# Kernel tuning notes

Hardware: AMD Instinct MI355X
Metric: run time of the kernel (lower is better)

Reference implementation:

```python
import jax, jax.numpy as jnp
import numpy as np

PS = 16
E = 512          # embed_dim
H = 8            # num_heads
EPS = 1e-5


def _ln(x, g, b):
    m = jnp.mean(x, axis=-1, keepdims=True)
    v = jnp.mean((x - m) ** 2, axis=-1, keepdims=True)
    return (x - m) * jax.lax.rsqrt(v + EPS) * g + b


def _mha(q_in, kv_in, in_w, in_b, out_w, out_b):
    # torch nn.MultiheadAttention: packed in_proj [3E, E], out_proj [E, E]
    Bq, Lq, _ = q_in.shape
    Lk = kv_in.shape[1]
    d = E // H
    wq, wk, wv = jnp.split(in_w, 3, axis=0)
    bq, bk, bv = jnp.split(in_b, 3, axis=0)
    q = (q_in @ wq.T + bq).reshape(Bq, Lq, H, d)
    k = (kv_in @ wk.T + bk).reshape(Bq, Lk, H, d)
    v = (kv_in @ wv.T + bv).reshape(Bq, Lk, H, d)
    scores = jnp.einsum('bqhd,bkhd->bhqk', q, k) / jnp.sqrt(jnp.float32(d))
    a = jax.nn.softmax(scores, axis=-1)
    o = jnp.einsum('bhqk,bkhd->bqhd', a, v).reshape(Bq, Lq, E)
    return o @ out_w.T + out_b


def setup_inputs() -> dict:
    key = jax.random.key(0)
    ks = jax.random.split(key, 24)
    s = 0.02
    D = 3 * PS * PS
    inp = {
        'neighbor_patches': jax.random.normal(ks[0], (8, 32, 32, 9, 3, PS, PS), jnp.float32),
        'w_pe': jax.random.normal(ks[1], (E, D), jnp.float32) * s,
        'b_pe': jnp.zeros((E,), jnp.float32),
        'pos_embed': jax.random.normal(ks[2], (1, 9, E), jnp.float32),
        'sa_in_w': jax.random.normal(ks[3], (3 * E, E), jnp.float32) * s,
        'sa_in_b': jnp.zeros((3 * E,), jnp.float32),
        'sa_out_w': jax.random.normal(ks[4], (E, E), jnp.float32) * s,
        'sa_out_b': jnp.zeros((E,), jnp.float32),
        'g1': jnp.ones((E,), jnp.float32), 'beta1': jnp.zeros((E,), jnp.float32),
        'ca_in_w': jax.random.normal(ks[5], (3 * E, E), jnp.float32) * s,
        'ca_in_b': jnp.zeros((3 * E,), jnp.float32),
        'ca_out_w': jax.random.normal(ks[6], (E, E), jnp.float32) * s,
        'ca_out_b': jnp.zeros((E,), jnp.float32),
        'g2': jnp.ones((E,), jnp.float32), 'beta2': jnp.zeros((E,), jnp.float32),
        'w1': jax.random.normal(ks[7], (4 * E, E), jnp.float32) * s,
        'b1': jnp.zeros((4 * E,), jnp.float32),
        'w2': jax.random.normal(ks[8], (E, 4 * E), jnp.float32) * s,
        'b2': jnp.zeros((E,), jnp.float32),
        'g3': jnp.ones((E,), jnp.float32), 'beta3': jnp.zeros((E,), jnp.float32),
    }
    return inp


def reference(neighbor_patches, w_pe, b_pe, pos_embed,
              sa_in_w, sa_in_b, sa_out_w, sa_out_b, g1, beta1,
              ca_in_w, ca_in_b, ca_out_w, ca_out_b, g2, beta2,
              w1, b1, w2, b2, g3, beta3):
    B, NH, NW, NN, C, ps, _ = neighbor_patches.shape
    x = neighbor_patches.reshape(B * NH * NW, NN, C * ps * ps)
    x = x @ w_pe.T + b_pe                       # [BN, 9, E]
    x = x + pos_embed
    attn = _mha(x, x, sa_in_w, sa_in_b, sa_out_w, sa_out_b)
    x = _ln(x + attn, g1, beta1)
    cq = x[:, 4:5, :]                            # center query [BN, 1, E]
    attn = _mha(cq, x, ca_in_w, ca_in_b, ca_out_w, ca_out_b)
    c = _ln(cq + attn, g2, beta2)
    ffn = jax.nn.gelu(c @ w1.T + b1, approximate=False) @ w2.T + b2
    out = _ln(c + ffn, g3, beta3)
    return out[:, 0, :].reshape(B, NH * NW, E)
```

## Files before the change

kernel.cpp:

```cpp
#include <hip/hip_runtime.h>


typedef unsigned short u16;
typedef u16   u16x8 __attribute__((ext_vector_type(8)));
typedef u16   u16x4 __attribute__((ext_vector_type(4)));
typedef __bf16 bf16x8 __attribute__((ext_vector_type(8)));
typedef float f32x4 __attribute__((ext_vector_type(4)));

static __device__ __forceinline__ u16 f2bf(float f) {
  union { float f; unsigned u; } v; v.f = f;
  unsigned r = v.u + 0x7FFFu + ((v.u >> 16) & 1u);
  return (u16)(r >> 16);
}
static __device__ __forceinline__ float bf2f(u16 u) {
  union { unsigned u; float f; } v; v.u = ((unsigned)u) << 16;
  return v.f;
}

static __device__ __forceinline__ void gld16(const void* g, void* l) {
  __builtin_amdgcn_global_load_lds(
      (__attribute__((address_space(1))) unsigned int*)(size_t)g,
      (__attribute__((address_space(3))) unsigned int*)(unsigned)(size_t)l,
      16, 0, 0);
}

static __device__ __forceinline__ int xcd_swz(int bid, int nwg) {
  int q = nwg >> 3, r = nwg & 7;
  int xcd = bid & 7, sub = bid >> 3;
  return (xcd < r ? xcd * (q + 1) : r * (q + 1) + (xcd - r) * q) + sub;
}

#define BAR   __builtin_amdgcn_s_barrier()
#define VM0   asm volatile("s_waitcnt vmcnt(0)" ::: "memory")
#define VM4   asm volatile("s_waitcnt vmcnt(4)" ::: "memory")

template<bool HAS_POS, bool HAS_RES, bool HAS_GELU>
__global__ __launch_bounds__(256, 3) void gemm_k2(
    const u16* __restrict__ A, int lda,
    const u16* __restrict__ W,
    const float* __restrict__ bias,
    const float* __restrict__ pos,
    const u16* res, int res_stride,
    u16* out,
    int M, int N, int K, int nbx)
{
  __shared__ u16 As[3][4096];
  __shared__ u16 Bs[3][4096];

  const int t    = threadIdx.x;
  const int lane = t & 63, wv = t >> 6;
  const int swz  = xcd_swz(blockIdx.x, gridDim.x);
  const int bm   = (swz / nbx) * 128, bn = (swz % nbx) * 128;
  const int wr   = wv >> 1, wc = wv & 1;

  const int srow = lane >> 2;
  const int skk  = (((lane & 3) ^ ((lane >> 3) & 3)) << 3);
  const int lr = lane & 15;
  const int rg = (((lane >> 4) ^ ((lr >> 1) & 3)) << 3);

  f32x4 acc[4][4] = {};

  auto stage = [&](int buf, int kt) {
    #pragma unroll
    for (int c = 0; c < 2; ++c) {
      int rr = (wv + 4 * c) * 16 + srow;
      gld16(A + (size_t)(bm + rr) * lda + kt * 32 + skk, &As[buf][(wv + 4 * c) * 512]);
      gld16(W + (size_t)(bn + rr) * K   + kt * 32 + skk, &Bs[buf][(wv + 4 * c) * 512]);
    }
  };

  const int nkt = K >> 5;
  stage(0, 0);
  stage(1, 1);
  VM4; BAR;

  int cur = 0, st = 2;
  for (int kt = 0; kt < nkt; ++kt) {
    if (kt + 2 < nkt) stage(st, kt + 2);

    bf16x8 a[4], b[4];
    #pragma unroll
    for (int m = 0; m < 4; ++m) {
      int row = wr * 64 + m * 16 + lr;
      a[m] = *(const bf16x8*)&As[cur][row * 32 + rg];
    }
    #pragma unroll
    for (int n = 0; n < 4; ++n) {
      int row = wc * 64 + n * 16 + lr;
      b[n] = *(const bf16x8*)&Bs[cur][row * 32 + rg];
    }
    #pragma unroll
    for (int m = 0; m < 4; ++m)
      #pragma unroll
      for (int n = 0; n < 4; ++n)
        acc[m][n] = __builtin_amdgcn_mfma_f32_16x16x32_bf16(a[m], b[n], acc[m][n], 0, 0, 0);

    if (kt + 2 < nkt) { VM4; } else { VM0; }
    BAR;
    cur = (cur == 2) ? 0 : cur + 1;
    st  = (st  == 2) ? 0 : st  + 1;
  }

  const int lq = lane >> 4;
  #pragma unroll
  for (int m = 0; m < 4; ++m) {
    #pragma unroll
    for (int n = 0; n < 4; ++n) {
      int col = bn + wc * 64 + n * 16 + lr;
      float bv = bias[col];
      #pragma unroll
      for (int r = 0; r < 4; ++r) {
        int row = bm + wr * 64 + m * 16 + lq * 4 + r;
        float v = acc[m][n][r] + bv;
        if constexpr (HAS_POS) v += pos[(row % 9) * 512 + col];
        if constexpr (HAS_RES) v += bf2f(res[(size_t)row * res_stride + col]);
        if constexpr (HAS_GELU) v = 0.5f * v * (1.f + erff(v * 0.70710678118f));
        out[(size_t)row * N + col] = f2bf(v);
      }
    }
  }
}

__global__ __launch_bounds__(256) void ln_k(
    const u16* in,
    const float* __restrict__ g, const float* __restrict__ be,
    u16* out_bf, float* out_f32, int rows)
{
  int wv = threadIdx.x >> 6, lane = threadIdx.x & 63;
  int row = blockIdx.x * 4 + wv;
  if (row >= rows) return;
  const u16* p = in + (size_t)row * 512;
  u16x8 v = *(const u16x8*)&p[lane * 8];
  float x[8], s = 0.f, sq = 0.f;
  #pragma unroll
  for (int j = 0; j < 8; ++j) { x[j] = bf2f(v[j]); s += x[j]; sq += x[j] * x[j]; }
  #pragma unroll
  for (int o = 32; o > 0; o >>= 1) { s += __shfl_xor(s, o, 64); sq += __shfl_xor(sq, o, 64); }
  float mean = s * (1.f / 512.f);
  float var  = sq * (1.f / 512.f) - mean * mean;
  float rs   = rsqrtf(var + 1e-5f);
  float y[8];
  #pragma unroll
  for (int j = 0; j < 8; ++j) {
    int c = lane * 8 + j;
    y[j] = (x[j] - mean) * rs * g[c] + be[c];
  }
  if (out_bf) {
    u16x8 o8;
    #pragma unroll
    for (int j = 0; j < 8; ++j) o8[j] = f2bf(y[j]);
    *(u16x8*)&out_bf[(size_t)row * 512 + lane * 8] = o8;
  }
  if (out_f32) {
    #pragma unroll
    for (int j = 0; j < 8; ++j) out_f32[(size_t)row * 512 + lane * 8 + j] = y[j];
  }
}

__global__ __launch_bounds__(256) void sa_attn_k(const u16* __restrict__ qkv,
                                                 u16* __restrict__ out)
{
  __shared__ u16  s_qkv[9 * 1536];
  __shared__ float s_sc[8][81];
  const int s = blockIdx.x, t = threadIdx.x;
  const u16* src = qkv + (size_t)s * 9 * 1536;
  for (int i = t; i < (9 * 1536) / 8; i += 256)
    *(u16x8*)&s_qkv[i * 8] = *(const u16x8*)&src[i * 8];
  __syncthreads();

  const int h = t >> 5, sl = t & 31;
  for (int p = sl; p < 81; p += 32) {
    int qi = p / 9, ki = p % 9;
    const u16* qp = &s_qkv[qi * 1536 + h * 64];
    const u16* kp = &s_qkv[ki * 1536 + 512 + h * 64];
    float d = 0.f;
    #pragma unroll
    for (int e8 = 0; e8 < 8; ++e8) {
      u16x8 qv = *(const u16x8*)&qp[e8 * 8];
      u16x8 kv = *(const u16x8*)&kp[e8 * 8];
      #pragma unroll
      for (int j = 0; j < 8; ++j) d += bf2f(qv[j]) * bf2f(kv[j]);
    }
    s_sc[h][p] = d * 0.125f;
  }
  __syncthreads();

  if (t < 72) {
    int hh = t / 9, qi = t % 9;
    float* sc = &s_sc[hh][qi * 9];
    float mx = sc[0];
    #pragma unroll
    for (int i = 1; i < 9; ++i) mx = fmaxf(mx, sc[i]);
    float e[9], sum = 0.f;
    #pragma unroll
    for (int i = 0; i < 9; ++i) { e[i] = __expf(sc[i] - mx); sum += e[i]; }
    float inv = 1.f / sum;
    #pragma unroll
    for (int i = 0; i < 9; ++i) sc[i] = e[i] * inv;
  }
  __syncthreads();

  for (int gidx = sl; gidx < 72; gidx += 32) {
    int qi = gidx >> 3, dg = gidx & 7;
    float a[8] = {};
    #pragma unroll
    for (int ki = 0; ki < 9; ++ki) {
      float pr = s_sc[h][qi * 9 + ki];
      u16x8 vv = *(const u16x8*)&s_qkv[ki * 1536 + 1024 + h * 64 + dg * 8];
      #pragma unroll
      for (int j = 0; j < 8; ++j) a[j] += pr * bf2f(vv[j]);
    }
    u16x8 o8;
    #pragma unroll
    for (int j = 0; j < 8; ++j) o8[j] = f2bf(a[j]);
    *(u16x8*)&out[((size_t)s * 9 + qi) * 512 + h * 64 + dg * 8] = o8;
  }
}

__global__ __launch_bounds__(256) void ca_attn_k(const u16* __restrict__ q,
                                                 const u16* __restrict__ kv,
                                                 u16* __restrict__ out)
{
  __shared__ u16  s_q[512];
  __shared__ u16  s_kv[9 * 1024];
  __shared__ float s_sc[8][9];
  const int s = blockIdx.x, t = threadIdx.x;
  if (t < 64) *(u16x8*)&s_q[t * 8] = *(const u16x8*)&q[(size_t)s * 512 + t * 8];
  for (int i = t; i < (9 * 1024) / 8; i += 256)
    *(u16x8*)&s_kv[i * 8] = *(const u16x8*)&kv[(size_t)s * 9 * 1024 + i * 8];
  __syncthreads();

  if (t < 72) {
    int h = t / 9, ki = t % 9;
    const u16* qp = &s_q[h * 64];
    const u16* kp = &s_kv[ki * 1024 + h * 64];
    float d = 0.f;
    #pragma unroll
    for (int e8 = 0; e8 < 8; ++e8) {
      u16x8 qv = *(const u16x8*)&qp[e8 * 8];
      u16x8 kvv = *(const u16x8*)&kp[e8 * 8];
      #pragma unroll
      for (int j = 0; j < 8; ++j) d += bf2f(qv[j]) * bf2f(kvv[j]);
    }
    s_sc[h][ki] = d * 0.125f;
  }
  __syncthreads();

  if (t < 8) {
    float* sc = s_sc[t];
    float mx = sc[0];
    #pragma unroll
    for (int i = 1; i < 9; ++i) mx = fmaxf(mx, sc[i]);
    float e[9], sum = 0.f;
    #pragma unroll
    for (int i = 0; i < 9; ++i) { e[i] = __expf(sc[i] - mx); sum += e[i]; }
    float inv = 1.f / sum;
    #pragma unroll
    for (int i = 0; i < 9; ++i) sc[i] = e[i] * inv;
  }
  __syncthreads();

  if (t < 64) {
    int h = t >> 3, dg = t & 7;
    float a[8] = {};
    #pragma unroll
    for (int ki = 0; ki < 9; ++ki) {
      float pr = s_sc[h][ki];
      u16x8 vv = *(const u16x8*)&s_kv[ki * 1024 + 512 + h * 64 + dg * 8];
      #pragma unroll
      for (int j = 0; j < 8; ++j) a[j] += pr * bf2f(vv[j]);
    }
    u16x8 o8;
    #pragma unroll
    for (int j = 0; j < 8; ++j) o8[j] = f2bf(a[j]);
    *(u16x8*)&out[(size_t)s * 512 + h * 64 + dg * 8] = o8;
  }
}

__global__ __launch_bounds__(256) void cvt_k(const float* __restrict__ in,
                                             u16* __restrict__ out, long n)
{
  long i = ((long)blockIdx.x * 256 + threadIdx.x) * 4;
  long stride = (long)gridDim.x * 1024;
  for (; i < n; i += stride) {
    float4 f = *(const float4*)&in[i];
    u16x4 o; o.x = f2bf(f.x); o.y = f2bf(f.y); o.z = f2bf(f.z); o.w = f2bf(f.w);
    *(u16x4*)&out[i] = o;
  }
}

extern "C" void kernel_launch(void* const* d_in, const int* in_sizes, int n_in,
                              void* d_out, int out_size, void* d_ws, size_t ws_size,
                              hipStream_t stream)
{
  const float* patches  = (const float*)d_in[0];
  const float* w_pe     = (const float*)d_in[1];
  const float* b_pe     = (const float*)d_in[2];
  const float* pos      = (const float*)d_in[3];
  const float* sa_in_w  = (const float*)d_in[4];
  const float* sa_in_b  = (const float*)d_in[5];
  const float* sa_out_w = (const float*)d_in[6];
  const float* sa_out_b = (const float*)d_in[7];
  const float* g1       = (const float*)d_in[8];
  const float* beta1    = (const float*)d_in[9];
  const float* ca_in_w  = (const float*)d_in[10];
  const float* ca_in_b  = (const float*)d_in[11];
  const float* ca_out_w = (const float*)d_in[12];
  const float* ca_out_b = (const float*)d_in[13];
  const float* g2       = (const float*)d_in[14];
  const float* beta2    = (const float*)d_in[15];
  const float* w1       = (const float*)d_in[16];
  const float* b1       = (const float*)d_in[17];
  const float* w2       = (const float*)d_in[18];
  const float* b2       = (const float*)d_in[19];
  const float* g3       = (const float*)d_in[20];
  const float* beta3    = (const float*)d_in[21];
  float* out = (float*)d_out;

  char* base = (char*)d_ws;
  u16* wbf        = (u16*)base;
  u16* w_pe_bf    = wbf;
  u16* sa_in_bf   = wbf + 393216;
  u16* sa_out_bf  = wbf + 1179648;
  u16* ca_in_bf   = wbf + 1441792;
  u16* ca_out_bf  = wbf + 2228224;
  u16* w1_bf      = wbf + 2490368;
  u16* w2_bf      = wbf + 3538944;
  u16* x_bf  = (u16*)(base + 9175040ull);
  u16* qkv   = (u16*)(base + 84672512ull);
  u16* pat_bf = qkv;
  u16* sattn = (u16*)(base + 311164928ull);
  u16* q_bf  = (u16*)(base + 386662400ull);
  u16* cattn = (u16*)(base + 395051008ull);
  u16* csum  = (u16*)(base + 403439616ull);
  u16* h_bf  = (u16*)(base + 411828224ull);
  u16* osum  = (u16*)(base + 445382656ull);

  cvt_k<<<2048, 256, 0, stream>>>(patches, pat_bf, 56623104L);
  cvt_k<<<384, 256, 0, stream>>>(w_pe, w_pe_bf, 393216L);
  cvt_k<<<768, 256, 0, stream>>>(sa_in_w, sa_in_bf, 786432L);
  cvt_k<<<256, 256, 0, stream>>>(sa_out_w, sa_out_bf, 262144L);
  cvt_k<<<768, 256, 0, stream>>>(ca_in_w, ca_in_bf, 786432L);
  cvt_k<<<256, 256, 0, stream>>>(ca_out_w, ca_out_bf, 262144L);
  cvt_k<<<1024, 256, 0, stream>>>(w1, w1_bf, 1048576L);
  cvt_k<<<1024, 256, 0, stream>>>(w2, w2_bf, 1048576L);

  gemm_k2<true, false, false><<<2304, 256, 0, stream>>>(
      pat_bf, 768, w_pe_bf, b_pe, pos, nullptr, 0, x_bf, 73728, 512, 768, 4);
  gemm_k2<false, false, false><<<6912, 256, 0, stream>>>(
      x_bf, 512, sa_in_bf, sa_in_b, nullptr, nullptr, 0, qkv, 73728, 1536, 512, 12);
  sa_attn_k<<<8192, 256, 0, stream>>>(qkv, sattn);
  gemm_k2<false, true, false><<<2304, 256, 0, stream>>>(
      sattn, 512, sa_out_bf, sa_out_b, nullptr, x_bf, 512, x_bf, 73728, 512, 512, 4);
  ln_k<<<73728 / 4, 256, 0, stream>>>(x_bf, g1, beta1, x_bf, nullptr, 73728);
  gemm_k2<false, false, false><<<256, 256, 0, stream>>>(
      x_bf + 2048, 4608, ca_in_bf, ca_in_b, nullptr, nullptr, 0, q_bf, 8192, 512, 512, 4);
  gemm_k2<false, false, false><<<4608, 256, 0, stream>>>(
      x_bf, 512, ca_in_bf + 262144, ca_in_b + 512, nullptr, nullptr, 0, qkv, 73728, 1024, 512, 8);
  ca_attn_k<<<8192, 256, 0, stream>>>(q_bf, qkv, cattn);
  gemm_k2<false, true, false><<<256, 256, 0, stream>>>(
      cattn, 512, ca_out_bf, ca_out_b, nullptr, x_bf + 2048, 4608, csum, 8192, 512, 512, 4);
  ln_k<<<8192 / 4, 256, 0, stream>>>(csum, g2, beta2, csum, nullptr, 8192);
  gemm_k2<false, false, true><<<1024, 256, 0, stream>>>(
      csum, 512, w1_bf, b1, nullptr, nullptr, 0, h_bf, 8192, 2048, 512, 16);
  gemm_k2<false, true, false><<<256, 256, 0, stream>>>(
      h_bf, 2048, w2_bf, b2, nullptr, csum, 512, osum, 8192, 512, 2048, 4);
  ln_k<<<8192 / 4, 256, 0, stream>>>(osum, g3, beta3, nullptr, out, 8192);
}
```

Before: 805.9 us.

## Add 128x256-tile GEMM with fused fp32-to-bf16 A conversion for patch embed

Introduces a wider 128x256 GEMM kernel in which each wave computes 64x128, and uses it for the large-M GEMMs: patch embed, the QKV projections, self-attention out-proj and FFN1. For patch embed it reads the fp32 patches directly into registers and converts them to bf16 while writing LDS. This removes the separate 113M-element conversion pass and its extra write and read of a bf16 copy. The wider tile raises B-operand reuse, at the cost of more accumulator registers (occupancy bound lowered to 2) and fewer blocks.

```diff
diff --git a/kernel.cpp b/kernel.cpp
--- a/kernel.cpp
+++ b/kernel.cpp
@@ -5,6 +5,7 @@
 typedef u16   u16x8 __attribute__((ext_vector_type(8)));
 typedef u16   u16x4 __attribute__((ext_vector_type(4)));
 typedef __bf16 bf16x8 __attribute__((ext_vector_type(8)));
+typedef __bf16 bf16x4 __attribute__((ext_vector_type(4)));
 typedef float f32x4 __attribute__((ext_vector_type(4)));
 
 static __device__ __forceinline__ u16 f2bf(float f) {
@@ -33,6 +34,139 @@
 #define BAR   __builtin_amdgcn_s_barrier()
 #define VM0   asm volatile("s_waitcnt vmcnt(0)" ::: "memory")
 #define VM4   asm volatile("s_waitcnt vmcnt(4)" ::: "memory")
+#define VM6   asm volatile("s_waitcnt vmcnt(6)" ::: "memory")
+#define LGKM0 asm volatile("s_waitcnt lgkmcnt(0)" ::: "memory")
+
+template<bool A_F32, bool HAS_POS, bool HAS_RES, bool HAS_GELU>
+__global__ __launch_bounds__(256, 2) void gemm_w(
+    const void* Av, int lda,
+    const u16* __restrict__ W,
+    const float* __restrict__ bias,
+    const float* __restrict__ pos,
+    const u16* res, int res_stride,
+    u16* out,
+    int M, int N, int K, int nbx)
+{
+  __shared__ u16 As[3][128 * 32];
+  __shared__ u16 Bs[3][256 * 32];
+
+  const int t    = threadIdx.x;
+  const int lane = t & 63, wv = t >> 6;
+  const int swz  = xcd_swz(blockIdx.x, gridDim.x);
+  const int bm   = (swz / nbx) * 128, bn = (swz % nbx) * 256;
+  const int wr   = wv >> 1, wc = wv & 1;
+
+  const int srow = lane >> 2;
+  const int skk  = (((lane & 3) ^ ((lane >> 3) & 3)) << 3);
+  const int lr   = lane & 15;
+  const int rg   = (((lane >> 4) ^ ((lr >> 1) & 3)) << 3);
+
+  f32x4 acc[4][8] = {};
+  float4 areg[4];
+
+  auto stageB = [&](int buf, int kt) {
+    #pragma unroll
+    for (int c = 0; c < 4; ++c) {
+      int rr = c * 64 + wv * 16;
+      gld16(W + (size_t)(bn + rr + srow) * K + kt * 32 + skk,
+            &Bs[buf][rr * 32]);
+    }
+  };
+  auto stageA16 = [&](int buf, int kt) {
+    const u16* A = (const u16*)Av;
+    #pragma unroll
+    for (int c = 0; c < 2; ++c) {
+      int rr = c * 64 + wv * 16;
+      gld16(A + (size_t)(bm + rr + srow) * lda + kt * 32 + skk,
+            &As[buf][rr * 32]);
+    }
+  };
+  auto loadAf32 = [&](int kt) {
+    const float* A = (const float*)Av;
+    #pragma unroll
+    for (int i = 0; i < 4; ++i) {
+      int idx = i * 256 + t, r = idx >> 3, c4 = (idx & 7) * 4;
+      areg[i] = *(const float4*)(A + (size_t)(bm + r) * lda + kt * 32 + c4);
+    }
+  };
+  auto writeAf32 = [&](int buf) {
+    #pragma unroll
+    for (int i = 0; i < 4; ++i) {
+      int idx = i * 256 + t, r = idx >> 3, c4 = (idx & 7) * 4;
+      int g = (c4 >> 3) ^ ((r >> 1) & 3);
+      int off = r * 32 + g * 8 + (c4 & 4);
+      bf16x4 h;
+      h.x = (__bf16)areg[i].x; h.y = (__bf16)areg[i].y;
+      h.z = (__bf16)areg[i].z; h.w = (__bf16)areg[i].w;
+      *(u16x4*)&As[buf][off] = *(u16x4*)&h;
+    }
+  };
+
+  const int nkt = K >> 5;
+  if constexpr (A_F32) {
+    loadAf32(0); stageB(0, 0);
+    VM4;  writeAf32(0);
+    loadAf32(1); stageB(1, 1);
+    VM4;  writeAf32(1);
+    LGKM0; BAR;
+  } else {
+    stageA16(0, 0); stageB(0, 0);
+    stageA16(1, 1); stageB(1, 1);
+    VM6; BAR;
+  }
+
+  int cur = 0, st = 2;
+  for (int kt = 0; kt < nkt; ++kt) {
+    const bool pf2 = (kt + 2 < nkt);
+    if (pf2) {
+      if constexpr (A_F32) { loadAf32(kt + 2); stageB(st, kt + 2); }
+      else                 { stageA16(st, kt + 2); stageB(st, kt + 2); }
+    }
+
+    bf16x8 a[4], b[8];
+    #pragma unroll
+    for (int m = 0; m < 4; ++m)
+      a[m] = *(const bf16x8*)&As[cur][(wr * 64 + m * 16 + lr) * 32 + rg];
+    #pragma unroll
+    for (int n = 0; n < 8; ++n)
+      b[n] = *(const bf16x8*)&Bs[cur][(wc * 128 + n * 16 + lr) * 32 + rg];
+    #pragma unroll
+    for (int m = 0; m < 4; ++m)
+      #pragma unroll
+      for (int n = 0; n < 8; ++n)
+        acc[m][n] = __builtin_amdgcn_mfma_f32_16x16x32_bf16(a[m], b[n], acc[m][n], 0, 0, 0);
+
+    if constexpr (A_F32) {
+      if (pf2) { VM4; writeAf32(st); }
+      else     { VM0; }
+      LGKM0; BAR;
+    } else {
+      if (pf2) { VM6; } else { VM0; }
+      BAR;
+    }
+    cur = (cur == 2) ? 0 : cur + 1;
+    st  = (st  == 2) ? 0 : st  + 1;
+  }
+
+  const int lq = lane >> 4;
+  #pragma unroll
+  for (int m = 0; m < 4; ++m) {
+    #pragma unroll
+    for (int n = 0; n < 8; ++n) {
+      int col = bn + wc * 128 + n * 16 + lr;
+      float bv = bias[col];
+      #pragma unroll
+      for (int r = 0; r < 4; ++r) {
+        int row = bm + wr * 64 + m * 16 + lq * 4 + r;
+        float v = acc[m][n][r] + bv;
+        if constexpr (HAS_POS) v += pos[(row % 9) * 512 + col];
+        if constexpr (HAS_RES) v += bf2f(res[(size_t)row * res_stride + col]);
+        if constexpr (HAS_GELU) v = 0.5f * v * (1.f + erff(v * 0.70710678118f));
+        out[(size_t)row * N + col] = f2bf(v);
+      }
+    }
+  }
+}
 
 template<bool HAS_POS, bool HAS_RES, bool HAS_GELU>
 __global__ __launch_bounds__(256, 3) void gemm_k2(
@@ -80,15 +214,11 @@
 
     bf16x8 a[4], b[4];
     #pragma unroll
-    for (int m = 0; m < 4; ++m) {
-      int row = wr * 64 + m * 16 + lr;
-      a[m] = *(const bf16x8*)&As[cur][row * 32 + rg];
-    }
-    #pragma unroll
-    for (int n = 0; n < 4; ++n) {
-      int row = wc * 64 + n * 16 + lr;
-      b[n] = *(const bf16x8*)&Bs[cur][row * 32 + rg];
-    }
+    for (int m = 0; m < 4; ++m)
+      a[m] = *(const bf16x8*)&As[cur][(wr * 64 + m * 16 + lr) * 32 + rg];
+    #pragma unroll
+    for (int n = 0; n < 4; ++n)
+      b[n] = *(const bf16x8*)&Bs[cur][(wc * 64 + n * 16 + lr) * 32 + rg];
     #pragma unroll
     for (int m = 0; m < 4; ++m)
       #pragma unroll
@@ -328,7 +458,6 @@
   u16* w2_bf      = wbf + 3538944;
   u16* x_bf  = (u16*)(base + 9175040ull);
   u16* qkv   = (u16*)(base + 84672512ull);
-  u16* pat_bf = qkv;
   u16* sattn = (u16*)(base + 311164928ull);
   u16* q_bf  = (u16*)(base + 386662400ull);
   u16* cattn = (u16*)(base + 395051008ull);
@@ -336,7 +465,6 @@
   u16* h_bf  = (u16*)(base + 411828224ull);
   u16* osum  = (u16*)(base + 445382656ull);
 
-  cvt_k<<<2048, 256, 0, stream>>>(patches, pat_bf, 56623104L);
   cvt_k<<<384, 256, 0, stream>>>(w_pe, w_pe_bf, 393216L);
   cvt_k<<<768, 256, 0, stream>>>(sa_in_w, sa_in_bf, 786432L);
   cvt_k<<<256, 256, 0, stream>>>(sa_out_w, sa_out_bf, 262144L);
@@ -345,24 +473,24 @@
   cvt_k<<<1024, 256, 0, stream>>>(w1, w1_bf, 1048576L);
   cvt_k<<<1024, 256, 0, stream>>>(w2, w2_bf, 1048576L);
 
-  gemm_k2<true, false, false><<<2304, 256, 0, stream>>>(
-      pat_bf, 768, w_pe_bf, b_pe, pos, nullptr, 0, x_bf, 73728, 512, 768, 4);
-  gemm_k2<false, false, false><<<6912, 256, 0, stream>>>(
-      x_bf, 512, sa_in_bf, sa_in_b, nullptr, nullptr, 0, qkv, 73728, 1536, 512, 12);
+  gemm_w<true, true, false, false><<<1152, 256, 0, stream>>>(
+      patches, 768, w_pe_bf, b_pe, pos, nullptr, 0, x_bf, 73728, 512, 768, 2);
+  gemm_w<false, false, false, false><<<3456, 256, 0, stream>>>(
+      x_bf, 512, sa_in_bf, sa_in_b, nullptr, nullptr, 0, qkv, 73728, 1536, 512, 6);
   sa_attn_k<<<8192, 256, 0, stream>>>(qkv, sattn);
-  gemm_k2<false, true, false><<<2304, 256, 0, stream>>>(
-      sattn, 512, sa_out_bf, sa_out_b, nullptr, x_bf, 512, x_bf, 73728, 512, 512, 4);
+  gemm_w<false, false, true, false><<<1152, 256, 0, stream>>>(
+      sattn, 512, sa_out_bf, sa_out_b, nullptr, x_bf, 512, x_bf, 73728, 512, 512, 2);
   ln_k<<<73728 / 4, 256, 0, stream>>>(x_bf, g1, beta1, x_bf, nullptr, 73728);
   gemm_k2<false, false, false><<<256, 256, 0, stream>>>(
       x_bf + 2048, 4608, ca_in_bf, ca_in_b, nullptr, nullptr, 0, q_bf, 8192, 512, 512, 4);
-  gemm_k2<false, false, false><<<4608, 256, 0, stream>>>(
-      x_bf, 512, ca_in_bf + 262144, ca_in_b + 512, nullptr, nullptr, 0, qkv, 73728, 1024, 512, 8);
+  gemm_w<false, false, false, false><<<2304, 256, 0, stream>>>(
+      x_bf, 512, ca_in_bf + 262144, ca_in_b + 512, nullptr, nullptr, 0, qkv, 73728, 1024, 512, 4);
   ca_attn_k<<<8192, 256, 0, stream>>>(q_bf, qkv, cattn);
   gemm_k2<false, true, false><<<256, 256, 0, stream>>>(
       cattn, 512, ca_out_bf, ca_out_b, nullptr, x_bf + 2048, 4608, csum, 8192, 512, 512, 4);
   ln_k<<<8192 / 4, 256, 0, stream>>>(csum, g2, beta2, csum, nullptr, 8192);
-  gemm_k2<false, false, true><<<1024, 256, 0, stream>>>(
-      csum, 512, w1_bf, b1, nullptr, nullptr, 0, h_bf, 8192, 2048, 512, 16);
+  gemm_w<false, false, false, true><<<512, 256, 0, stream>>>(
+      csum, 512, w1_bf, b1, nullptr, nullptr, 0, h_bf, 8192, 2048, 512, 8);
   gemm_k2<false, true, false><<<256, 256, 0, stream>>>(
       h_bf, 2048, w2_bf, b2, nullptr, csum, 512, osum, 8192, 512, 2048, 4);
   ln_k<<<8192 / 4, 256, 0, stream>>>(osum, g3, beta3, nullptr, out, 8192);
```

After: 825.9 us. +2.5%, slower.

## Fuse fp32 patch conversion into patch-embed GEMM and batch weight conversions

Applied to the files above, without the earlier changes.

The patch-embedding GEMM now reads the fp32 patches directly into registers, converts them to bf16 and writes them into swizzled LDS, instead of first running a separate conversion pass that writes a bf16 copy. This removes one full write and re-read of the largest tensor. The seven weight conversion launches are merged into one kernel that picks the source tensor by block index. In exchange, the A-operand loads in the fused GEMM now go through registers rather than direct global-to-LDS loads, which adds register pressure and LDS write/wait latency to that GEMM's pipeline.

```diff
diff --git a/kernel.cpp b/kernel.cpp
--- a/kernel.cpp
+++ b/kernel.cpp
@@ -5,6 +5,7 @@
 typedef u16   u16x8 __attribute__((ext_vector_type(8)));
 typedef u16   u16x4 __attribute__((ext_vector_type(4)));
 typedef __bf16 bf16x8 __attribute__((ext_vector_type(8)));
+typedef __bf16 bf16x4 __attribute__((ext_vector_type(4)));
 typedef float f32x4 __attribute__((ext_vector_type(4)));
 
 static __device__ __forceinline__ u16 f2bf(float f) {
@@ -32,11 +33,13 @@
 
 #define BAR   __builtin_amdgcn_s_barrier()
 #define VM0   asm volatile("s_waitcnt vmcnt(0)" ::: "memory")
+#define VM2   asm volatile("s_waitcnt vmcnt(2)" ::: "memory")
 #define VM4   asm volatile("s_waitcnt vmcnt(4)" ::: "memory")
-
-template<bool HAS_POS, bool HAS_RES, bool HAS_GELU>
+#define LGKM0 asm volatile("s_waitcnt lgkmcnt(0)" ::: "memory")
+
+template<bool A_F32, bool HAS_POS, bool HAS_RES, bool HAS_GELU>
 __global__ __launch_bounds__(256, 3) void gemm_k2(
-    const u16* __restrict__ A, int lda,
+    const void* Av, int lda,
     const u16* __restrict__ W,
     const float* __restrict__ bias,
     const float* __restrict__ pos,
@@ -59,8 +62,10 @@
   const int rg = (((lane >> 4) ^ ((lr >> 1) & 3)) << 3);
 
   f32x4 acc[4][4] = {};
+  float4 areg[4];
 
   auto stage = [&](int buf, int kt) {
+    const u16* A = (const u16*)Av;
     #pragma unroll
     for (int c = 0; c < 2; ++c) {
       int rr = (wv + 4 * c) * 16 + srow;
@@ -68,35 +73,75 @@
       gld16(W + (size_t)(bn + rr) * K   + kt * 32 + skk, &Bs[buf][(wv + 4 * c) * 512]);
     }
   };
+  auto stageB = [&](int buf, int kt) {
+    #pragma unroll
+    for (int c = 0; c < 2; ++c) {
+      int rr = (wv + 4 * c) * 16 + srow;
+      gld16(W + (size_t)(bn + rr) * K + kt * 32 + skk, &Bs[buf][(wv + 4 * c) * 512]);
+    }
+  };
+  auto loadAf32 = [&](int kt) {
+    const float* A = (const float*)Av;
+    #pragma unroll
+    for (int i = 0; i < 4; ++i) {
+      int idx = i * 256 + t, r = idx >> 3, c4 = (idx & 7) * 4;
+      areg[i] = *(const float4*)(A + (size_t)(bm + r) * lda + kt * 32 + c4);
+    }
+  };
+  auto writeAf32 = [&](int buf) {
+    #pragma unroll
+    for (int i = 0; i < 4; ++i) {
+      int idx = i * 256 + t, r = idx >> 3, c4 = (idx & 7) * 4;
+      int g = (c4 >> 3) ^ ((r >> 1) & 3);
+      int off = r * 32 + g * 8 + (c4 & 4);
+      bf16x4 h;
+      h.x = (__bf16)areg[i].x; h.y = (__bf16)areg[i].y;
+      h.z = (__bf16)areg[i].z; h.w = (__bf16)areg[i].w;
+      *(u16x4*)&As[buf][off] = *(u16x4*)&h;
+    }
+  };
 
   const int nkt = K >> 5;
-  stage(0, 0);
-  stage(1, 1);
-  VM4; BAR;
+  if constexpr (A_F32) {
+    loadAf32(0); stageB(0, 0);
+    VM2;  writeAf32(0);
+    loadAf32(1); stageB(1, 1);
+    VM2;  writeAf32(1);
+    LGKM0; BAR;
+  } else {
+    stage(0, 0);
+    stage(1, 1);
+    VM4; BAR;
+  }
 
   int cur = 0, st = 2;
   for (int kt = 0; kt < nkt; ++kt) {
-    if (kt + 2 < nkt) stage(st, kt + 2);
+    const bool pf2 = (kt + 2 < nkt);
+    if (pf2) {
+      if constexpr (A_F32) { loadAf32(kt + 2); stageB(st, kt + 2); }
+      else                 { stage(st, kt + 2); }
+    }
 
     bf16x8 a[4], b[4];
     #pragma unroll
-    for (int m = 0; m < 4; ++m) {
-      int row = wr * 64 + m * 16 + lr;
-      a[m] = *(const bf16x8*)&As[cur][row * 32 + rg];
-    }
-    #pragma unroll
-    for (int n = 0; n < 4; ++n) {
-      int row = wc * 64 + n * 16 + lr;
-      b[n] = *(const bf16x8*)&Bs[cur][row * 32 + rg];
-    }
+    for (int m = 0; m < 4; ++m)
+      a[m] = *(const bf16x8*)&As[cur][(wr * 64 + m * 16 + lr) * 32 + rg];
+    #pragma unroll
+    for (int n = 0; n < 4; ++n)
+      b[n] = *(const bf16x8*)&Bs[cur][(wc * 64 + n * 16 + lr) * 32 + rg];
     #pragma unroll
     for (int m = 0; m < 4; ++m)
       #pragma unroll
       for (int n = 0; n < 4; ++n)
         acc[m][n] = __builtin_amdgcn_mfma_f32_16x16x32_bf16(a[m], b[n], acc[m][n], 0, 0, 0);
 
-    if (kt + 2 < nkt) { VM4; } else { VM0; }
-    BAR;
+    if constexpr (A_F32) {
+      if (pf2) { VM2; writeAf32(st); } else { VM0; }
+      LGKM0; BAR;
+    } else {
+      if (pf2) { VM4; } else { VM0; }
+      BAR;
+    }
     cur = (cur == 2) ? 0 : cur + 1;
     st  = (st  == 2) ? 0 : st  + 1;
   }
@@ -277,16 +322,32 @@
   }
 }
 
-__global__ __launch_bounds__(256) void cvt_k(const float* __restrict__ in,
-                                             u16* __restrict__ out, long n)
-{
-  long i = ((long)blockIdx.x * 256 + threadIdx.x) * 4;
-  long stride = (long)gridDim.x * 1024;
-  for (; i < n; i += stride) {
-    float4 f = *(const float4*)&in[i];
-    u16x4 o; o.x = f2bf(f.x); o.y = f2bf(f.y); o.z = f2bf(f.z); o.w = f2bf(f.w);
-    *(u16x4*)&out[i] = o;
-  }
+__global__ __launch_bounds__(256) void wcvt_k(
+    const float* s0, const float* s1, const float* s2, const float* s3,
+    const float* s4, const float* s5, const float* s6, u16* dst)
+{
+  int b = blockIdx.x;
+  const float* sp; long base;
+  if      (b < 384)  { sp = s0; base = 0;       }
+  else if (b < 1152) { sp = s1; base = 393216;  }
+  else if (b < 1408) { sp = s2; base = 1179648; }
+  else if (b < 2176) { sp = s3; base = 1441792; }
+  else if (b < 2432) { sp = s4; base = 2228224; }
+  else if (b < 3456) { sp = s5; base = 2490368; }
+  else               { sp = s6; base = 3538944; }
+  long loc = ((long)b * 1024 - base * 0) ;
+  long segStart;
+  if      (b < 384)  segStart = 0;
+  else if (b < 1152) segStart = 384;
+  else if (b < 1408) segStart = 1152;
+  else if (b < 2176) segStart = 1408;
+  else if (b < 2432) segStart = 2176;
+  else if (b < 3456) segStart = 2432;
+  else               segStart = 3456;
+  loc = ((long)b - segStart) * 1024 + (long)threadIdx.x * 4;
+  float4 f = *(const float4*)(sp + loc);
+  u16x4 o; o.x = f2bf(f.x); o.y = f2bf(f.y); o.z = f2bf(f.z); o.w = f2bf(f.w);
+  *(u16x4*)&dst[base + loc] = o;
 }
 
 extern "C" void kernel_launch(void* const* d_in, const int* in_sizes, int n_in,
@@ -328,7 +389,6 @@
   u16* w2_bf      = wbf + 3538944;
   u16* x_bf  = (u16*)(base + 9175040ull);
   u16* qkv   = (u16*)(base + 84672512ull);
-  u16* pat_bf = qkv;
   u16* sattn = (u16*)(base + 311164928ull);
   u16* q_bf  = (u16*)(base + 386662400ull);
   u16* cattn = (u16*)(base + 395051008ull);
@@ -336,34 +396,28 @@
   u16* h_bf  = (u16*)(base + 411828224ull);
   u16* osum  = (u16*)(base + 445382656ull);
 
-  cvt_k<<<2048, 256, 0, stream>>>(patches, pat_bf, 56623104L);
-  cvt_k<<<384, 256, 0, stream>>>(w_pe, w_pe_bf, 393216L);
-  cvt_k<<<768, 256, 0, stream>>>(sa_in_w, sa_in_bf, 786432L);
-  cvt_k<<<256, 256, 0, stream>>>(sa_out_w, sa_out_bf, 262144L);
-  cvt_k<<<768, 256, 0, stream>>>(ca_in_w, ca_in_bf, 786432L);
-  cvt_k<<<256, 256, 0, stream>>>(ca_out_w, ca_out_bf, 262144L);
-  cvt_k<<<1024, 256, 0, stream>>>(w1, w1_bf, 1048576L);
-  cvt_k<<<1024, 256, 0, stream>>>(w2, w2_bf, 1048576L);
-
-  gemm_k2<true, false, false><<<2304, 256, 0, stream>>>(
-      pat_bf, 768, w_pe_bf, b_pe, pos, nullptr, 0, x_bf, 73728, 512, 768, 4);
-  gemm_k2<false, false, false><<<6912, 256, 0, stream>>>(
+  wcvt_k<<<4480, 256, 0, stream>>>(w_pe, sa_in_w, sa_out_w, ca_in_w,
+                                   ca_out_w, w1, w2, wbf);
+
+  gemm_k2<true, true, false, false><<<2304, 256, 0, stream>>>(
+      patches, 768, w_pe_bf, b_pe, pos, nullptr, 0, x_bf, 73728, 512, 768, 4);
+  gemm_k2<false, false, false, false><<<6912, 256, 0, stream>>>(
       x_bf, 512, sa_in_bf, sa_in_b, nullptr, nullptr, 0, qkv, 73728, 1536, 512, 12);
   sa_attn_k<<<8192, 256, 0, stream>>>(qkv, sattn);
-  gemm_k2<false, true, false><<<2304, 256, 0, stream>>>(
+  gemm_k2<false, false, true, false><<<2304, 256, 0, stream>>>(
       sattn, 512, sa_out_bf, sa_out_b, nullptr, x_bf, 512, x_bf, 73728, 512, 512, 4);
   ln_k<<<73728 / 4, 256, 0, stream>>>(x_bf, g1, beta1, x_bf, nullptr, 73728);
-  gemm_k2<false, false, false><<<256, 256, 0, stream>>>(
+  gemm_k2<false, false, false, false><<<256, 256, 0, stream>>>(
       x_bf + 2048, 4608, ca_in_bf, ca_in_b, nullptr, nullptr, 0, q_bf, 8192, 512, 512, 4);
-  gemm_k2<false, false, false><<<4608, 256, 0, stream>>>(
+  gemm_k2<false, false, false, false><<<4608, 256, 0, stream>>>(
       x_bf, 512, ca_in_bf + 262144, ca_in_b + 512, nullptr, nullptr, 0, qkv, 73728, 1024, 512, 8);
   ca_attn_k<<<8192, 256, 0, stream>>>(q_bf, qkv, cattn);
-  gemm_k2<false, true, false><<<256, 256, 0, stream>>>(
+  gemm_k2<false, false, true, false><<<256, 256, 0, stream>>>(
       cattn, 512, ca_out_bf, ca_out_b, nullptr, x_bf + 2048, 4608, csum, 8192, 512, 512, 4);
   ln_k<<<8192 / 4, 256, 0, stream>>>(csum, g2, beta2, csum, nullptr, 8192);
-  gemm_k2<false, false, true><<<1024, 256, 0, stream>>>(
+  gemm_k2<false, false, false, true><<<1024, 256, 0, stream>>>(
       csum, 512, w1_bf, b1, nullptr, nullptr, 0, h_bf, 8192, 2048, 512, 16);
-  gemm_k2<false, true, false><<<256, 256, 0, stream>>>(
+  gemm_k2<false, false, true, false><<<256, 256, 0, stream>>>(
       h_bf, 2048, w2_bf, b2, nullptr, csum, 512, osum, 8192, 512, 2048, 4);
   ln_k<<<8192 / 4, 256, 0, stream>>>(osum, g3, beta3, nullptr, out, 8192);
 }
```

Result: faster. 779.6 us (-3.3%).
